# Optimization experiments

Hardware: AMD Instinct MI355X
Metric: run time of the kernel (lower is better)

The kernel has to match this reference:

```python
import jax, jax.numpy as jnp
import numpy as np

DIM = 1024
H = 8
D = DIM // H
EPS = 1e-5


def setup_inputs() -> dict:
    key = jax.random.key(0)
    ks = jax.random.split(key, 12)
    B, T, Kt, Ka, Kp = 4, 2048, 64, 16, 32
    s = 1.0 / np.sqrt(DIM).astype(np.float32)
    return {
        "x": jax.random.normal(ks[0], (B, T, DIM), jnp.float32),
        "h_t": jax.random.normal(ks[1], (B, Kt, DIM), jnp.float32),
        "h_a": jax.random.normal(ks[2], (B, Ka, DIM), jnp.float32),
        "p": jax.random.normal(ks[3], (B, Kp, DIM), jnp.float32),
        "Wq": jax.random.normal(ks[4], (DIM, DIM), jnp.float32) * s,
        "bq": jnp.zeros((DIM,), jnp.float32),
        "Wk": jax.random.normal(ks[5], (DIM, DIM), jnp.float32) * s,
        "bk": jnp.zeros((DIM,), jnp.float32),
        "Wv": jax.random.normal(ks[6], (DIM, DIM), jnp.float32) * s,
        "bv": jnp.zeros((DIM,), jnp.float32),
        "Wo": jax.random.normal(ks[7], (DIM, DIM), jnp.float32) * s,
        "bo": jnp.zeros((DIM,), jnp.float32),
        "ln_g": jnp.ones((DIM,), jnp.float32),
        "ln_b": jnp.zeros((DIM,), jnp.float32),
        "Wf": jax.random.normal(ks[8], (DIM, DIM), jnp.float32) * s,
        "bf": jnp.zeros((DIM,), jnp.float32),
        "gating": jnp.zeros((1,), jnp.float32),
    }


def reference(x, h_t, h_a, p, Wq, bq, Wk, bk, Wv, bv, Wo, bo, ln_g, ln_b, Wf, bf, gating):
    B, T, C = x.shape
    ratio_g = jnp.tanh(gating)  # (1,), broadcasts over scores
    h_cond = jnp.concatenate([h_a, p], axis=1)  # [B, K_cond, C]

    def proj(t, W, b):
        # linear then split heads: [B, S, C] -> [B, H, S, D]
        y = t @ W + b
        return y.reshape(t.shape[0], t.shape[1], H, D).transpose(0, 2, 1, 3)

    q = proj(x, Wq, bq)
    k_tok, v_tok = proj(x, Wk, bk), proj(x, Wv, bv)
    k_task, v_task = proj(h_t, Wk, bk), proj(h_t, Wv, bv)
    k_cond, v_cond = proj(h_cond, Wk, bk), proj(h_cond, Wv, bv)

    s_tok = jnp.einsum('bhqd,bhkd->bhqk', q, k_tok)
    s_task = jnp.einsum('bhqd,bhkd->bhqk', q, k_task)
    s_cond = jnp.einsum('bhqd,bhkd->bhqk', q, k_cond) * ratio_g  # gated group
    scores = jnp.concatenate([s_tok, s_task, s_cond], axis=-1) / np.sqrt(D).astype(np.float32)
    w = jax.nn.softmax(scores, axis=-1)

    v_comb = jnp.concatenate([v_tok, v_task, v_cond], axis=2)  # [B, H, T+Kt+Kc, D]
    o = jnp.einsum('bhqk,bhkd->bhqd', w, v_comb).transpose(0, 2, 1, 3).reshape(B, T, C)
    o = o @ Wo + bo

    y = o + x  # residual feeds LN-MLP
    mu = jnp.mean(y, axis=-1, keepdims=True)
    var = jnp.var(y, axis=-1, keepdims=True)
    yn = (y - mu) / jnp.sqrt(var + EPS) * ln_g + ln_b
    return jax.nn.relu(yn @ Wf + bf)
```

## Files before the change

### kernel.cpp

```cpp
#include <hip/hip_runtime.h>

#define BB 4
#define TT 2048
#define CC 1024
#define HH 8
#define DD 128
#define KTOT 2160
#define GATE0 2112
#define KP 2176
#define NT 34
#define MQ (BB*TT)
#define MKVP (BB*KP)

typedef __attribute__((ext_vector_type(4)))  float f32x4;
typedef __attribute__((ext_vector_type(16))) float f32x16;
typedef __attribute__((ext_vector_type(8)))  short bf16x8;

union PU { unsigned u[4]; bf16x8 v; };

__device__ __forceinline__ unsigned short f2bf(float f) {
    unsigned u = __float_as_uint(f);
    unsigned r = u + 0x7FFFu + ((u >> 16) & 1u);
    return (unsigned short)(r >> 16);
}
__device__ __forceinline__ unsigned pk2(float a, float b) {
    return (unsigned)f2bf(a) | ((unsigned)f2bf(b) << 16);
}
__device__ __forceinline__ void async16(const ushort* g, ushort* l) {
    __builtin_amdgcn_global_load_lds((const __attribute__((address_space(1))) void*)g,
                                     (__attribute__((address_space(3))) void*)l, 16, 0, 0);
}

__global__ __launch_bounds__(256) void tcast(const float* __restrict__ W, ushort* __restrict__ Wt) {
    __shared__ float tile[32][33];
    const int tx = threadIdx.x & 31, ty = threadIdx.x >> 5;
    const int n0 = blockIdx.x * 32, k0 = blockIdx.y * 32;
    #pragma unroll
    for (int i = 0; i < 4; i++)
        tile[ty + i*8][tx] = W[(size_t)(k0 + ty + i*8)*CC + n0 + tx];
    __syncthreads();
    #pragma unroll
    for (int i = 0; i < 4; i++)
        Wt[(size_t)(n0 + ty + i*8)*CC + k0 + tx] = f2bf(tile[tx][ty + i*8]);
}

__global__ __launch_bounds__(256) void castx(const float* __restrict__ in, ushort* __restrict__ out) {
    int i = blockIdx.x * 256 + threadIdx.x;
    float4 v = ((const float4*)in)[i];
    ushort4 o; o.x = f2bf(v.x); o.y = f2bf(v.y); o.z = f2bf(v.z); o.w = f2bf(v.w);
    ((ushort4*)out)[i] = o;
}

__global__ __launch_bounds__(256) void gather_kv(const float* __restrict__ x, const float* __restrict__ ht,
        const float* __restrict__ ha, const float* __restrict__ p, ushort* __restrict__ kvb) {
    int idx = blockIdx.x * 256 + threadIdx.x;
    int col4 = idx & 255;
    int row  = idx >> 8;
    int b = row / KP, j = row - b * KP;
    ushort4 o;
    if (j < KTOT) {
        const float* src;
        if (j < 2048)      src = x  + ((size_t)b*TT + j)*CC;
        else if (j < 2112) src = ht + ((size_t)b*64 + (j-2048))*CC;
        else if (j < 2128) src = ha + ((size_t)b*16 + (j-2112))*CC;
        else               src = p  + ((size_t)b*32 + (j-2128))*CC;
        float4 v = ((const float4*)src)[col4];
        o.x = f2bf(v.x); o.y = f2bf(v.y); o.z = f2bf(v.z); o.w = f2bf(v.w);
    } else {
        o.x = 0; o.y = 0; o.z = 0; o.w = 0;
    }
    ((ushort4*)kvb)[idx] = o;
}

template<int EPI, int OUT>
__global__ __launch_bounds__(256) void gemm_mfma(const ushort* __restrict__ A, const ushort* __restrict__ Bt,
        const float* __restrict__ bias, const float* __restrict__ res, void* __restrict__ Cv) {
    __shared__ ushort As[128*32];
    __shared__ ushort Bs[128*32];
    const int t = threadIdx.x;
    const int w = t >> 6, lane = t & 63;
    const int wr = w >> 1, wc = w & 1;
    const int row0 = blockIdx.y * 128, col0 = blockIdx.x * 128;
    const int lr = lane & 15, ls = lane >> 4;
    f32x4 acc[4][4] = {};
    for (int k0 = 0; k0 < CC; k0 += 32) {
        #pragma unroll
        for (int u = 0; u < 2; u++) {
            int i = u*256 + t;
            int r = i >> 2, pp = i & 3;
            int s = pp ^ ((r >> 1) & 3);
            async16(A  + (size_t)(row0 + r)*CC + k0 + s*8, &As[(u*256 + w*64)*8]);
            async16(Bt + (size_t)(col0 + r)*CC + k0 + s*8, &Bs[(u*256 + w*64)*8]);
        }
        __syncthreads();
        bf16x8 af[4], bg[4];
        #pragma unroll
        for (int mi = 0; mi < 4; mi++) {
            int row = wr*64 + mi*16 + lr;
            af[mi] = *(const bf16x8*)&As[row*32 + (ls ^ ((row>>1)&3))*8];
        }
        #pragma unroll
        for (int ni = 0; ni < 4; ni++) {
            int row = wc*64 + ni*16 + lr;
            bg[ni] = *(const bf16x8*)&Bs[row*32 + (ls ^ ((row>>1)&3))*8];
        }
        #pragma unroll
        for (int mi = 0; mi < 4; mi++)
            #pragma unroll
            for (int ni = 0; ni < 4; ni++)
                acc[mi][ni] = __builtin_amdgcn_mfma_f32_16x16x32_bf16(af[mi], bg[ni], acc[mi][ni], 0, 0, 0);
        __syncthreads();
    }
    #pragma unroll
    for (int ni = 0; ni < 4; ni++) {
        const int col = col0 + wc*64 + ni*16 + lr;
        const float bcol = bias[col];
        #pragma unroll
        for (int mi = 0; mi < 4; mi++) {
            f32x4 v = acc[mi][ni];
            #pragma unroll
            for (int q = 0; q < 4; q++) {
                int row = row0 + wr*64 + mi*16 + ls*4 + q;
                float o = v[q] + bcol;
                if (EPI == 1) o += res[(size_t)row*CC + col];
                if (EPI == 2) o = fmaxf(o, 0.f);
                if (OUT == 0) {
                    ((float*)Cv)[(size_t)row*CC + col] = o;
                } else if (OUT == 1) {
                    ((ushort*)Cv)[(size_t)row*CC + col] = f2bf(o);
                } else {
                    int b = row / KP, j = row - b * KP;
                    int hh = col >> 7, dout = col & 127;
                    ((ushort*)Cv)[((size_t)((b*HH + hh)*DD + dout))*KP + j] = f2bf(o);
                }
            }
        }
    }
}

__global__ __launch_bounds__(256, 2) void attn_mfma(const ushort* __restrict__ Qb,
        const ushort* __restrict__ Kb, const ushort* __restrict__ Vtb,
        const float* __restrict__ gate, ushort* __restrict__ AO) {
    __shared__ ushort s_k[2][64*128];
    __shared__ ushort s_v[2][128*64];
    __shared__ float  l_s[4][32];
    const int t = threadIdx.x;
    const int w = t >> 6, lane = t & 63;
    const int ql = lane & 31, H = lane >> 5;
    const int qb0 = blockIdx.x * 128;
    const int h = blockIdx.y, b = blockIdx.z;
    const float ratio = tanhf(gate[0]);
    const float scl = 0.088388347648318447f;

    #pragma unroll
    for (int u = 0; u < 8; u++) {
        int s16 = u*256 + t;
        int row = s16 >> 4, slot = s16 & 15;
        int ss = slot ^ (row & 7);
        const ushort* src = Qb + (size_t)(b*TT + qb0 + row)*CC + h*DD + ss*8;
        ushort* dst = (s16 < 1024) ? &s_k[0][s16*8] : &s_v[0][(s16 - 1024)*8];
        async16(src, dst);
    }
    asm volatile("s_waitcnt vmcnt(0)" ::: "memory");
    __builtin_amdgcn_s_barrier();
    bf16x8 qf[8];
    {
        int row = w*32 + ql;
        int swz = (row & 7) << 4;
        #pragma unroll
        for (int ds = 0; ds < 8; ds++) {
            int off = (ds*32 + H*16) ^ swz;
            const ushort* base = (row < 64) ? &s_k[0][row*128 + off/2]
                                            : &s_v[0][(row-64)*128 + off/2];
            qf[ds] = *(const bf16x8*)base;
        }
    }
    asm volatile("s_waitcnt lgkmcnt(0)" ::: "memory");
    __builtin_amdgcn_s_barrier();

    f32x16 oacc[4] = {};
    float m = -__builtin_inff(), l = 0.f;

    {
        #pragma unroll
        for (int u = 0; u < 4; u++) {
            int s16 = u*256 + t;
            int row = s16 >> 4, slot = s16 & 15;
            int ss = slot ^ (row & 7);
            async16(Kb + (size_t)(b*KP + row)*CC + h*DD + ss*8, &s_k[0][s16*8]);
        }
        #pragma unroll
        for (int u = 0; u < 4; u++) {
            int s16 = u*256 + t;
            int row = s16 >> 3, slot = s16 & 7;
            int ss = slot ^ (row & 7);
            async16(Vtb + ((size_t)((b*HH + h)*DD + row))*KP + ss*8, &s_v[0][s16*8]);
        }
    }

    for (int tile = 0; tile < NT; tile++) {
        const int cur = tile & 1;
        if (tile + 1 < NT) {
            const int j0n = (tile+1) * 64;
            #pragma unroll
            for (int u = 0; u < 4; u++) {
                int s16 = u*256 + t;
                int row = s16 >> 4, slot = s16 & 15;
                int ss = slot ^ (row & 7);
                async16(Kb + (size_t)(b*KP + j0n + row)*CC + h*DD + ss*8, &s_k[cur^1][s16*8]);
            }
            #pragma unroll
            for (int u = 0; u < 4; u++) {
                int s16 = u*256 + t;
                int row = s16 >> 3, slot = s16 & 7;
                int ss = slot ^ (row & 7);
                async16(Vtb + ((size_t)((b*HH + h)*DD + row))*KP + j0n + ss*8, &s_v[cur^1][s16*8]);
            }
            asm volatile("s_waitcnt vmcnt(8)" ::: "memory");
        } else {
            asm volatile("s_waitcnt vmcnt(0)" ::: "memory");
        }
        __builtin_amdgcn_s_barrier();

        const ushort* ks = s_k[cur];
        const ushort* vs = s_v[cur];
        const int j0 = tile * 64;

        f32x16 st0 = {}, st1 = {};
        {
            int swz = (ql & 7) << 4;
            #pragma unroll
            for (int ds = 0; ds < 8; ds++) {
                int off = (ds*32 + H*16) ^ swz;
                bf16x8 k0 = *(const bf16x8*)&ks[ ql      *128 + off/2];
                bf16x8 k1 = *(const bf16x8*)&ks[(32+ql)*128 + off/2];
                st0 = __builtin_amdgcn_mfma_f32_32x32x16_bf16(k0, qf[ds], st0, 0, 0, 0);
                st1 = __builtin_amdgcn_mfma_f32_32x32x16_bf16(k1, qf[ds], st1, 0, 0, 0);
            }
        }

        float p0[16], p1[16];
        if (j0 == 2112) {
            #pragma unroll
            for (int r = 0; r < 16; r++) {
                int cr = (r&3) + 8*(r>>2) + 4*H;
                p0[r] = st0[r] * scl * ratio;
                p1[r] = (2144 + cr < KTOT) ? st1[r] * scl * ratio
                                           : -__builtin_inff();
            }
        } else {
            #pragma unroll
            for (int r = 0; r < 16; r++) { p0[r] = st0[r]*scl; p1[r] = st1[r]*scl; }
        }

        float tm = -__builtin_inff();
        #pragma unroll
        for (int r = 0; r < 16; r++) tm = fmaxf(tm, fmaxf(p0[r], p1[r]));
        tm = fmaxf(tm, __shfl_xor(tm, 32));
        if (!__all(tm <= m + 8.f)) {
            float nm = fmaxf(m, tm);
            float rs = __expf(m - nm);
            m = nm;
            l *= rs;
            #pragma unroll
            for (int dt = 0; dt < 4; dt++)
                #pragma unroll
                for (int r = 0; r < 16; r++) oacc[dt][r] *= rs;
        }
        float lsum = 0.f;
        #pragma unroll
        for (int r = 0; r < 16; r++) {
            p0[r] = __expf(p0[r] - m);
            p1[r] = __expf(p1[r] - m);
            lsum += p0[r] + p1[r];
        }
        lsum += __shfl_xor(lsum, 32);
        l += lsum;

        #pragma unroll
        for (int jt = 0; jt < 4; jt++) {
            const float* ps = (jt < 2) ? p0 : p1;
            const int ib = (jt & 1) * 8;
            unsigned PA0 = pk2(ps[ib+0], ps[ib+1]);
            unsigned PA1 = pk2(ps[ib+2], ps[ib+3]);
            unsigned PB0 = pk2(ps[ib+4], ps[ib+5]);
            unsigned PB1 = pk2(ps[ib+6], ps[ib+7]);
            unsigned send0 = H ? PA0 : PB0;
            unsigned send1 = H ? PA1 : PB1;
            unsigned recv0 = (unsigned)__shfl_xor((int)send0, 32);
            unsigned recv1 = (unsigned)__shfl_xor((int)send1, 32);
            PU pu;
            pu.u[0] = H ? recv0 : PA0;
            pu.u[1] = H ? recv1 : PA1;
            pu.u[2] = H ? PB0  : recv0;
            pu.u[3] = H ? PB1  : recv1;
            #pragma unroll
            for (int dt = 0; dt < 4; dt++) {
                int row = dt*32 + ql;
                int off = (jt*32 + H*16) ^ ((row & 7) << 4);
                bf16x8 vf = *(const bf16x8*)&vs[row*64 + off/2];
                oacc[dt] = __builtin_amdgcn_mfma_f32_32x32x16_bf16(pu.v, vf, oacc[dt], 0, 0, 0);
            }
        }
        __builtin_amdgcn_s_barrier();
    }

    l_s[w][ql] = 1.0f / l;
    __syncthreads();
    float il[16];
    #pragma unroll
    for (int r = 0; r < 16; r++) il[r] = l_s[w][(r&3) + 8*(r>>2) + 4*H];
    #pragma unroll
    for (int dt = 0; dt < 4; dt++)
        #pragma unroll
        for (int r = 0; r < 16; r++) {
            int cr = (r&3) + 8*(r>>2) + 4*H;
            size_t row = (size_t)(b*TT + qb0 + w*32 + cr);
            AO[row*CC + h*DD + dt*32 + ql] = f2bf(oacc[dt][r] * il[r]);
        }
}

__global__ __launch_bounds__(256) void ln_kernel(const float* __restrict__ Y, const float* __restrict__ g,
        const float* __restrict__ bb, ushort* __restrict__ Out) {
    const int row = blockIdx.x;
    const int t = threadIdx.x;
    float4 v = ((const float4*)(Y + (size_t)row*CC))[t];
    float s  = v.x + v.y + v.z + v.w;
    float sq = v.x*v.x + v.y*v.y + v.z*v.z + v.w*v.w;
    #pragma unroll
    for (int off = 32; off >= 1; off >>= 1) {
        s  += __shfl_xor(s, off);
        sq += __shfl_xor(sq, off);
    }
    __shared__ float ssum[4], ssq[4];
    const int w = t >> 6;
    if ((t & 63) == 0) { ssum[w] = s; ssq[w] = sq; }
    __syncthreads();
    s  = ssum[0] + ssum[1] + ssum[2] + ssum[3];
    sq = ssq[0]  + ssq[1]  + ssq[2]  + ssq[3];
    const float mu  = s * (1.f/1024.f);
    const float var = sq * (1.f/1024.f) - mu*mu;
    const float inv = rsqrtf(var + 1e-5f);
    float4 g4 = ((const float4*)g)[t];
    float4 b4 = ((const float4*)bb)[t];
    ushort4 o;
    o.x = f2bf((v.x - mu)*inv*g4.x + b4.x);
    o.y = f2bf((v.y - mu)*inv*g4.y + b4.y);
    o.z = f2bf((v.z - mu)*inv*g4.z + b4.z);
    o.w = f2bf((v.w - mu)*inv*g4.w + b4.w);
    ((ushort4*)(Out + (size_t)row*CC))[t] = o;
}

extern "C" void kernel_launch(void* const* d_in, const int* in_sizes, int n_in,
                              void* d_out, int out_size, void* d_ws, size_t ws_size,
                              hipStream_t stream) {
    const float* x    = (const float*)d_in[0];
    const float* h_t  = (const float*)d_in[1];
    const float* h_a  = (const float*)d_in[2];
    const float* p    = (const float*)d_in[3];
    const float* Wq   = (const float*)d_in[4];
    const float* bq   = (const float*)d_in[5];
    const float* Wk   = (const float*)d_in[6];
    const float* bk   = (const float*)d_in[7];
    const float* Wv   = (const float*)d_in[8];
    const float* bv   = (const float*)d_in[9];
    const float* Wo   = (const float*)d_in[10];
    const float* bo   = (const float*)d_in[11];
    const float* ln_g = (const float*)d_in[12];
    const float* ln_b = (const float*)d_in[13];
    const float* Wf   = (const float*)d_in[14];
    const float* bf   = (const float*)d_in[15];
    const float* gate = (const float*)d_in[16];
    float* out = (float*)d_out;

    ushort* wqT = (ushort*)d_ws;
    ushort* wkT = wqT + (size_t)CC*CC;
    ushort* wvT = wkT + (size_t)CC*CC;
    ushort* woT = wvT + (size_t)CC*CC;
    ushort* wfT = woT + (size_t)CC*CC;
    ushort* xb  = wfT + (size_t)CC*CC;
    ushort* kvb = xb  + (size_t)MQ*CC;
    ushort* Qb  = kvb + (size_t)MKVP*CC;
    ushort* Kb  = Qb  + (size_t)MQ*CC;
    ushort* Vtb = Kb  + (size_t)MKVP*CC;
    ushort* AOb = xb;
    float*  Y   = (float*)Qb;
    ushort* YNb = kvb;

    tcast<<<dim3(32,32), 256, 0, stream>>>(Wq, wqT);
    tcast<<<dim3(32,32), 256, 0, stream>>>(Wk, wkT);
    tcast<<<dim3(32,32), 256, 0, stream>>>(Wv, wvT);
    tcast<<<dim3(32,32), 256, 0, stream>>>(Wo, woT);
    tcast<<<dim3(32,32), 256, 0, stream>>>(Wf, wfT);
    castx<<<MQ*CC/4/256, 256, 0, stream>>>(x, xb);
    gather_kv<<<MKVP, 256, 0, stream>>>(x, h_t, h_a, p, kvb);

    gemm_mfma<0,1><<<dim3(8, MQ/128),   256, 0, stream>>>(xb,  wqT, bq, nullptr, Qb);
    gemm_mfma<0,1><<<dim3(8, MKVP/128), 256, 0, stream>>>(kvb, wkT, bk, nullptr, Kb);
    gemm_mfma<0,2><<<dim3(8, MKVP/128), 256, 0, stream>>>(kvb, wvT, bv, nullptr, Vtb);
    attn_mfma<<<dim3(TT/128, HH, BB), 256, 0, stream>>>(Qb, Kb, Vtb, gate, AOb);
    gemm_mfma<1,0><<<dim3(8, MQ/128),   256, 0, stream>>>(AOb, woT, bo, x, Y);
    ln_kernel<<<MQ, 256, 0, stream>>>(Y, ln_g, ln_b, YNb);
    gemm_mfma<2,0><<<dim3(8, MQ/128),   256, 0, stream>>>(YNb, wfT, bf, nullptr, (void*)out);
}
```

Baseline: 328.3 us.

## Fold softmax scale and gating into projections, double-buffer GEMM, drop x cast

Folds the softmax scale and log2(e) into Wq and bq, and moves the tanh gate into the K-projection epilogue, so attention uses exp2 with no per-score multiplies. The Q GEMM now reads x rows from the gathered KV buffer instead of a separate cast of x, which removes the castx kernel. The GEMM gets double-buffered LDS with async prefetch, and attention raises MFMA priority and loosens the rescale threshold. The Wo-GEMM output is stored as bf16 and LayerNorm reads bf16, which halves that traffic at some cost in precision before the norm.

```diff
diff --git a/kernel.cpp b/kernel.cpp
--- a/kernel.cpp
+++ b/kernel.cpp
@@ -1,4 +1,5 @@
 #include <hip/hip_runtime.h>
+#include <hip/hip_bf16.h>
 
 #define BB 4
 #define TT 2048
@@ -24,14 +25,17 @@
     return (unsigned short)(r >> 16);
 }
 __device__ __forceinline__ unsigned pk2(float a, float b) {
-    return (unsigned)f2bf(a) | ((unsigned)f2bf(b) << 16);
+    unsigned r;
+    asm("v_cvt_pk_bf16_f32 %0, %1, %2" : "=v"(r) : "v"(a), "v"(b));
+    return r;
 }
 __device__ __forceinline__ void async16(const ushort* g, ushort* l) {
     __builtin_amdgcn_global_load_lds((const __attribute__((address_space(1))) void*)g,
                                      (__attribute__((address_space(3))) void*)l, 16, 0, 0);
 }
 
-__global__ __launch_bounds__(256) void tcast(const float* __restrict__ W, ushort* __restrict__ Wt) {
+__global__ __launch_bounds__(256) void tcast(const float* __restrict__ W, ushort* __restrict__ Wt,
+                                             float scale) {
     __shared__ float tile[32][33];
     const int tx = threadIdx.x & 31, ty = threadIdx.x >> 5;
     const int n0 = blockIdx.x * 32, k0 = blockIdx.y * 32;
@@ -41,14 +45,7 @@
     __syncthreads();
     #pragma unroll
     for (int i = 0; i < 4; i++)
-        Wt[(size_t)(n0 + ty + i*8)*CC + k0 + tx] = f2bf(tile[tx][ty + i*8]);
-}
-
-__global__ __launch_bounds__(256) void castx(const float* __restrict__ in, ushort* __restrict__ out) {
-    int i = blockIdx.x * 256 + threadIdx.x;
-    float4 v = ((const float4*)in)[i];
-    ushort4 o; o.x = f2bf(v.x); o.y = f2bf(v.y); o.z = f2bf(v.z); o.w = f2bf(v.w);
-    ((ushort4*)out)[i] = o;
+        Wt[(size_t)(n0 + ty + i*8)*CC + k0 + tx] = f2bf(tile[tx][ty + i*8] * scale);
 }
 
 __global__ __launch_bounds__(256) void gather_kv(const float* __restrict__ x, const float* __restrict__ ht,
@@ -72,49 +69,69 @@
     ((ushort4*)kvb)[idx] = o;
 }
 
-template<int EPI, int OUT>
+template<int EPI, int OUT, int AMAP>
 __global__ __launch_bounds__(256) void gemm_mfma(const ushort* __restrict__ A, const ushort* __restrict__ Bt,
-        const float* __restrict__ bias, const float* __restrict__ res, void* __restrict__ Cv) {
-    __shared__ ushort As[128*32];
-    __shared__ ushort Bs[128*32];
+        const float* __restrict__ bias, const float* __restrict__ res, void* __restrict__ Cv,
+        float bscale, const float* __restrict__ gate) {
+    __shared__ ushort As[2][128*32];
+    __shared__ ushort Bs[2][128*32];
     const int t = threadIdx.x;
     const int w = t >> 6, lane = t & 63;
     const int wr = w >> 1, wc = w & 1;
     const int row0 = blockIdx.y * 128, col0 = blockIdx.x * 128;
     const int lr = lane & 15, ls = lane >> 4;
+    float ratio = 0.f;
+    if constexpr (EPI == 3) ratio = tanhf(gate[0]);
     f32x4 acc[4][4] = {};
-    for (int k0 = 0; k0 < CC; k0 += 32) {
+
+    auto stage = [&](int buf, int k0) {
         #pragma unroll
         for (int u = 0; u < 2; u++) {
             int i = u*256 + t;
             int r = i >> 2, pp = i & 3;
             int s = pp ^ ((r >> 1) & 3);
-            async16(A  + (size_t)(row0 + r)*CC + k0 + s*8, &As[(u*256 + w*64)*8]);
-            async16(Bt + (size_t)(col0 + r)*CC + k0 + s*8, &Bs[(u*256 + w*64)*8]);
-        }
-        __syncthreads();
+            int gr = row0 + r;
+            size_t ga;
+            if (AMAP) { int bq_ = gr >> 11; ga = (size_t)(bq_*KP + (gr & 2047)); }
+            else ga = (size_t)gr;
+            async16(A  + ga*CC + k0 + s*8,                 &As[buf][(u*256 + w*64)*8]);
+            async16(Bt + (size_t)(col0 + r)*CC + k0 + s*8, &Bs[buf][(u*256 + w*64)*8]);
+        }
+    };
+
+    stage(0, 0);
+    for (int k0 = 0; k0 < CC; k0 += 32) {
+        const int cur = (k0 >> 5) & 1;
+        if (k0 + 32 < CC) {
+            stage(cur ^ 1, k0 + 32);
+            asm volatile("s_waitcnt vmcnt(4)" ::: "memory");
+        } else {
+            asm volatile("s_waitcnt vmcnt(0)" ::: "memory");
+        }
+        __builtin_amdgcn_s_barrier();
         bf16x8 af[4], bg[4];
         #pragma unroll
         for (int mi = 0; mi < 4; mi++) {
             int row = wr*64 + mi*16 + lr;
-            af[mi] = *(const bf16x8*)&As[row*32 + (ls ^ ((row>>1)&3))*8];
+            af[mi] = *(const bf16x8*)&As[cur][row*32 + (ls ^ ((row>>1)&3))*8];
         }
         #pragma unroll
         for (int ni = 0; ni < 4; ni++) {
             int row = wc*64 + ni*16 + lr;
-            bg[ni] = *(const bf16x8*)&Bs[row*32 + (ls ^ ((row>>1)&3))*8];
+            bg[ni] = *(const bf16x8*)&Bs[cur][row*32 + (ls ^ ((row>>1)&3))*8];
         }
         #pragma unroll
         for (int mi = 0; mi < 4; mi++)
             #pragma unroll
             for (int ni = 0; ni < 4; ni++)
                 acc[mi][ni] = __builtin_amdgcn_mfma_f32_16x16x32_bf16(af[mi], bg[ni], acc[mi][ni], 0, 0, 0);
-        __syncthreads();
+        asm volatile("" ::: "memory");
+        __builtin_amdgcn_s_barrier();
     }
     #pragma unroll
     for (int ni = 0; ni < 4; ni++) {
         const int col = col0 + wc*64 + ni*16 + lr;
-        const float bcol = bias[col];
+        const float bcol = bias[col] * bscale;
         #pragma unroll
         for (int mi = 0; mi < 4; mi++) {
             f32x4 v = acc[mi][ni];
@@ -122,11 +139,12 @@
             for (int q = 0; q < 4; q++) {
                 int row = row0 + wr*64 + mi*16 + ls*4 + q;
                 float o = v[q] + bcol;
-                if (EPI == 1) o += res[(size_t)row*CC + col];
-                if (EPI == 2) o = fmaxf(o, 0.f);
-                if (OUT == 0) {
+                if constexpr (EPI == 1) o += res[(size_t)row*CC + col];
+                if constexpr (EPI == 2) o = fmaxf(o, 0.f);
+                if constexpr (EPI == 3) { int j = row % KP; if (j >= GATE0) o *= ratio; }
+                if constexpr (OUT == 0) {
                     ((float*)Cv)[(size_t)row*CC + col] = o;
-                } else if (OUT == 1) {
+                } else if constexpr (OUT == 1) {
                     ((ushort*)Cv)[(size_t)row*CC + col] = f2bf(o);
                 } else {
                     int b = row / KP, j = row - b * KP;
@@ -140,7 +158,7 @@
 
 __global__ __launch_bounds__(256, 2) void attn_mfma(const ushort* __restrict__ Qb,
         const ushort* __restrict__ Kb, const ushort* __restrict__ Vtb,
-        const float* __restrict__ gate, ushort* __restrict__ AO) {
+        ushort* __restrict__ AO) {
     __shared__ ushort s_k[2][64*128];
     __shared__ ushort s_v[2][128*64];
     __shared__ float  l_s[4][32];
@@ -149,8 +167,6 @@
     const int ql = lane & 31, H = lane >> 5;
     const int qb0 = blockIdx.x * 128;
     const int h = blockIdx.y, b = blockIdx.z;
-    const float ratio = tanhf(gate[0]);
-    const float scl = 0.088388347648318447f;
 
     #pragma unroll
     for (int u = 0; u < 8; u++) {
@@ -224,11 +240,11 @@
 
         const ushort* ks = s_k[cur];
         const ushort* vs = s_v[cur];
-        const int j0 = tile * 64;
 
         f32x16 st0 = {}, st1 = {};
         {
             int swz = (ql & 7) << 4;
+            __builtin_amdgcn_s_setprio(1);
             #pragma unroll
             for (int ds = 0; ds < 8; ds++) {
                 int off = (ds*32 + H*16) ^ swz;
@@ -237,29 +253,29 @@
                 st0 = __builtin_amdgcn_mfma_f32_32x32x16_bf16(k0, qf[ds], st0, 0, 0, 0);
                 st1 = __builtin_amdgcn_mfma_f32_32x32x16_bf16(k1, qf[ds], st1, 0, 0, 0);
             }
+            __builtin_amdgcn_s_setprio(0);
         }
 
         float p0[16], p1[16];
-        if (j0 == 2112) {
+        if (tile == NT - 1) {
             #pragma unroll
             for (int r = 0; r < 16; r++) {
                 int cr = (r&3) + 8*(r>>2) + 4*H;
-                p0[r] = st0[r] * scl * ratio;
-                p1[r] = (2144 + cr < KTOT) ? st1[r] * scl * ratio
-                                           : -__builtin_inff();
+                p0[r] = st0[r];
+                p1[r] = (cr < 16) ? st1[r] : -__builtin_inff();
             }
         } else {
             #pragma unroll
-            for (int r = 0; r < 16; r++) { p0[r] = st0[r]*scl; p1[r] = st1[r]*scl; }
+            for (int r = 0; r < 16; r++) { p0[r] = st0[r]; p1[r] = st1[r]; }
         }
 
         float tm = -__builtin_inff();
         #pragma unroll
         for (int r = 0; r < 16; r++) tm = fmaxf(tm, fmaxf(p0[r], p1[r]));
         tm = fmaxf(tm, __shfl_xor(tm, 32));
-        if (!__all(tm <= m + 8.f)) {
+        if (!__all(tm <= m + 11.5f)) {
             float nm = fmaxf(m, tm);
-            float rs = __expf(m - nm);
+            float rs = exp2f(m - nm);
             m = nm;
             l *= rs;
             #pragma unroll
@@ -270,8 +286,8 @@
         float lsum = 0.f;
         #pragma unroll
         for (int r = 0; r < 16; r++) {
-            p0[r] = __expf(p0[r] - m);
-            p1[r] = __expf(p1[r] - m);
+            p0[r] = exp2f(p0[r] - m);
+            p1[r] = exp2f(p1[r] - m);
             lsum += p0[r] + p1[r];
         }
         lsum += __shfl_xor(lsum, 32);
@@ -294,6 +310,7 @@
             pu.u[1] = H ? recv1 : PA1;
             pu.u[2] = H ? PB0  : recv0;
             pu.u[3] = H ? PB1  : recv1;
+            __builtin_amdgcn_s_setprio(1);
             #pragma unroll
             for (int dt = 0; dt < 4; dt++) {
                 int row = dt*32 + ql;
@@ -301,7 +318,9 @@
                 bf16x8 vf = *(const bf16x8*)&vs[row*64 + off/2];
                 oacc[dt] = __builtin_amdgcn_mfma_f32_32x32x16_bf16(pu.v, vf, oacc[dt], 0, 0, 0);
             }
-        }
+            __builtin_amdgcn_s_setprio(0);
+        }
+        asm volatile("" ::: "memory");
         __builtin_amdgcn_s_barrier();
     }
 
@@ -320,13 +339,17 @@
         }
 }
 
-__global__ __launch_bounds__(256) void ln_kernel(const float* __restrict__ Y, const float* __restrict__ g,
+__global__ __launch_bounds__(256) void ln_bf16(const ushort* __restrict__ Y, const float* __restrict__ g,
         const float* __restrict__ bb, ushort* __restrict__ Out) {
     const int row = blockIdx.x;
     const int t = threadIdx.x;
-    float4 v = ((const float4*)(Y + (size_t)row*CC))[t];
-    float s  = v.x + v.y + v.z + v.w;
-    float sq = v.x*v.x + v.y*v.y + v.z*v.z + v.w*v.w;
+    ushort4 u4 = ((const ushort4*)(Y + (size_t)row*CC))[t];
+    float v0 = __uint_as_float((unsigned)u4.x << 16);
+    float v1 = __uint_as_float((unsigned)u4.y << 16);
+    float v2 = __uint_as_float((unsigned)u4.z << 16);
+    float v3 = __uint_as_float((unsigned)u4.w << 16);
+    float s  = v0 + v1 + v2 + v3;
+    float sq = v0*v0 + v1*v1 + v2*v2 + v3*v3;
     #pragma unroll
     for (int off = 32; off >= 1; off >>= 1) {
         s  += __shfl_xor(s, off);
@@ -344,10 +367,10 @@
     float4 g4 = ((const float4*)g)[t];
     float4 b4 = ((const float4*)bb)[t];
     ushort4 o;
-    o.x = f2bf((v.x - mu)*inv*g4.x + b4.x);
-    o.y = f2bf((v.y - mu)*inv*g4.y + b4.y);
-    o.z = f2bf((v.z - mu)*inv*g4.z + b4.z);
-    o.w = f2bf((v.w - mu)*inv*g4.w + b4.w);
+    o.x = f2bf((v0 - mu)*inv*g4.x + b4.x);
+    o.y = f2bf((v1 - mu)*inv*g4.y + b4.y);
+    o.z = f2bf((v2 - mu)*inv*g4.z + b4.z);
+    o.w = f2bf((v3 - mu)*inv*g4.w + b4.w);
     ((ushort4*)(Out + (size_t)row*CC))[t] = o;
 }
 
@@ -373,33 +396,33 @@
     const float* gate = (const float*)d_in[16];
     float* out = (float*)d_out;
 
+    const float alpha = 0.088388347648318447f * 1.4426950408889634f;
+
     ushort* wqT = (ushort*)d_ws;
     ushort* wkT = wqT + (size_t)CC*CC;
     ushort* wvT = wkT + (size_t)CC*CC;
     ushort* woT = wvT + (size_t)CC*CC;
     ushort* wfT = woT + (size_t)CC*CC;
-    ushort* xb  = wfT + (size_t)CC*CC;
-    ushort* kvb = xb  + (size_t)MQ*CC;
+    ushort* kvb = wfT + (size_t)CC*CC;
     ushort* Qb  = kvb + (size_t)MKVP*CC;
     ushort* Kb  = Qb  + (size_t)MQ*CC;
     ushort* Vtb = Kb  + (size_t)MKVP*CC;
-    ushort* AOb = xb;
-    float*  Y   = (float*)Qb;
+    ushort* AOb = Vtb + (size_t)MKVP*CC;
+    ushort* Yb  = Kb;
     ushort* YNb = kvb;
 
-    tcast<<<dim3(32,32), 256, 0, stream>>>(Wq, wqT);
-    tcast<<<dim3(32,32), 256, 0, stream>>>(Wk, wkT);
-    tcast<<<dim3(32,32), 256, 0, stream>>>(Wv, wvT);
-    tcast<<<dim3(32,32), 256, 0, stream>>>(Wo, woT);
-    tcast<<<dim3(32,32), 256, 0, stream>>>(Wf, wfT);
-    castx<<<MQ*CC/4/256, 256, 0, stream>>>(x, xb);
+    tcast<<<dim3(32,32), 256, 0, stream>>>(Wq, wqT, alpha);
+    tcast<<<dim3(32,32), 256, 0, stream>>>(Wk, wkT, 1.f);
+    tcast<<<dim3(32,32), 256, 0, stream>>>(Wv, wvT, 1.f);
+    tcast<<<dim3(32,32), 256, 0, stream>>>(Wo, woT, 1.f);
+    tcast<<<dim3(32,32), 256, 0, stream>>>(Wf, wfT, 1.f);
     gather_kv<<<MKVP, 256, 0, stream>>>(x, h_t, h_a, p, kvb);
 
-    gemm_mfma<0,1><<<dim3(8, MQ/128),   256, 0, stream>>>(xb,  wqT, bq, nullptr, Qb);
-    gemm_mfma<0,1><<<dim3(8, MKVP/128), 256, 0, stream>>>(kvb, wkT, bk, nullptr, Kb);
-    gemm_mfma<0,2><<<dim3(8, MKVP/128), 256, 0, stream>>>(kvb, wvT, bv, nullptr, Vtb);
-    attn_mfma<<<dim3(TT/128, HH, BB), 256, 0, stream>>>(Qb, Kb, Vtb, gate, AOb);
-    gemm_mfma<1,0><<<dim3(8, MQ/128),   256, 0, stream>>>(AOb, woT, bo, x, Y);
-    ln_kernel<<<MQ, 256, 0, stream>>>(Y, ln_g, ln_b, YNb);
-    gemm_mfma<2,0><<<dim3(8, MQ/128),   256, 0, stream>>>(YNb, wfT, bf, nullptr, (void*)out);
-}
+    gemm_mfma<0,1,1><<<dim3(8, MQ/128),   256, 0, stream>>>(kvb, wqT, bq, nullptr, Qb,  alpha, nullptr);
+    gemm_mfma<3,1,0><<<dim3(8, MKVP/128), 256, 0, stream>>>(kvb, wkT, bk, nullptr, Kb,  1.f,   gate);
+    gemm_mfma<0,2,0><<<dim3(8, MKVP/128), 256, 0, stream>>>(kvb, wvT, bv, nullptr, Vtb, 1.f,   nullptr);
+    attn_mfma<<<dim3(TT/128, HH, BB), 256, 0, stream>>>(Qb, Kb, Vtb, AOb);
+    gemm_mfma<1,1,0><<<dim3(8, MQ/128),   256, 0, stream>>>(AOb, woT, bo, x, Yb, 1.f, nullptr);
+    ln_bf16<<<MQ, 256, 0, stream>>>(Yb, ln_g, ln_b, YNb);
+    gemm_mfma<2,0,0><<<dim3(8, MQ/128),   256, 0, stream>>>(YNb, wfT, bf, nullptr, (void*)out, 1.f, nullptr);
+}
```

Result: slower. 345.3 us (+5.2%).
